# Kernel optimization log

Measured on AMD Instinct MI355X. Metric: run time of the kernel, lower is better.

The kernel has to match this reference:

```python
import jax, jax.numpy as jnp
import numpy as np

B, N, D, P = 4, 512, 512, 128

def setup_inputs() -> dict:
    key = jax.random.key(0)
    ks = jax.random.split(key, 8)
    s = lambda fan_in: 1.0 / np.sqrt(fan_in)
    inp = {
        "input": jax.random.normal(ks[0], (B, N, D), dtype=jnp.float32),
        # bigram projections (weights stored [in, out]; torch Linear is [out, in])
        "Wl": jax.random.uniform(ks[1], (D, P), jnp.float32, -s(D), s(D)),
        "bl": jnp.zeros((P,), jnp.float32),  # zeroed in initialize_parameters
        "Wr": jax.random.uniform(ks[2], (D, P), jnp.float32, -s(D), s(D)),  # no bias
        "Wo": jax.random.uniform(ks[3], (P, 1), jnp.float32, -s(P), s(P)),
        "bo": jnp.zeros((1,), jnp.float32),
        # start builder MLP
        "Ws1": jax.random.uniform(ks[4], (D, P), jnp.float32, -s(D), s(D)),
        "bs1": jnp.zeros((P,), jnp.float32),
        "Ws2": jax.random.uniform(ks[5], (P, 1), jnp.float32, -s(P), s(P)),
        "bs2": jnp.zeros((1,), jnp.float32),
        # end builder MLP
        "We1": jax.random.uniform(ks[6], (D, P), jnp.float32, -s(D), s(D)),
        "be1": jnp.zeros((P,), jnp.float32),
        "We2": jax.random.uniform(ks[7], (P, 1), jnp.float32, -s(P), s(P)),
        "be2": jnp.zeros((1,), jnp.float32),
    }
    return inp


def reference(input, Wl, bl, Wr, Wo, bo, Ws1, bs1, Ws2, bs2, We1, be1, We2, be2):
    # start / end unigram scores: [B, N, 1]
    start = jnp.maximum(input @ Ws1 + bs1, 0.0) @ Ws2 + bs2
    end = jnp.maximum(input @ We1 + be1, 0.0) @ We2 + be2
    # bigram scores
    left = input @ Wl + bl   # [B, N, P]
    right = input @ Wr       # [B, N, P]
    # left.unsqueeze(1) + right.unsqueeze(2) -> [B, N, N, P]
    proj = left[:, None, :, :] + right[:, :, None, :]
    bigram = jnp.maximum(proj, 0.0) @ Wo + bo  # [B, N, N, 1]
    return (bigram, start, end)
```

## Files before the change

kernel.cpp:

```cpp
#include <hip/hip_runtime.h>

typedef unsigned short ushort_t;
using f32x4  = __attribute__((ext_vector_type(4))) float;
using bf16x8 = __attribute__((ext_vector_type(8))) short;
using u16x8  = __attribute__((ext_vector_type(8))) unsigned short;
using h2v    = __attribute__((ext_vector_type(2))) _Float16;

constexpr int Bc = 4;
constexpr int Nc = 512;
constexpr int Dc = 512;
constexpr int Pc = 128;
constexpr int ROWS = Bc * Nc;

__device__ inline unsigned short f2bf(float f) {
    unsigned u = __builtin_bit_cast(unsigned, f);
    unsigned r = u + 0x7fffu + ((u >> 16) & 1u);
    return (unsigned short)(r >> 16);
}

__device__ inline void gload_lds16(const void* g, void* l) {
    __builtin_amdgcn_global_load_lds(
        (const __attribute__((address_space(1))) unsigned int*)g,
        (__attribute__((address_space(3))) unsigned int*)l, 16, 0, 0);
}

__device__ inline unsigned packh2(float a, float b) {
    unsigned short lo = __builtin_bit_cast(unsigned short, (_Float16)a);
    unsigned short hi = __builtin_bit_cast(unsigned short, (_Float16)b);
    return (unsigned)lo | ((unsigned)hi << 16);
}

__global__ __launch_bounds__(256) void wconv_kernel(
    const float* __restrict__ Wl,  const float* __restrict__ Wr,
    const float* __restrict__ Ws1, const float* __restrict__ We1,
    ushort_t* __restrict__ WcatT2)
{
    const int bx = blockIdx.x, t = threadIdx.x;
    __shared__ float T[64][68];

    const int nt = bx >> 3, ks = bx & 7;
    const int mi = nt >> 1, cm0 = (nt & 1) * 64;
    const float* Wm = (mi == 0) ? Wl : (mi == 1) ? Wr : (mi == 2) ? Ws1 : We1;

    const int kk_ = t >> 4, cc = (t & 15) << 2;
    #pragma unroll
    for (int u = 0; u < 4; ++u)
        *(float4*)&T[kk_ + 16 * u][cc] =
            *(const float4*)&Wm[(size_t)(ks * 64 + kk_ + 16 * u) * Pc + cm0 + cc];
    __syncthreads();

    const int col = t & 63, c2 = t >> 6;
    #pragma unroll
    for (int h = 0; h < 2; ++h) {
        const int kc = c2 + h * 4;
        u16x8 o;
        #pragma unroll
        for (int i = 0; i < 8; ++i) o[i] = f2bf(T[kc * 8 + i][col]);
        *(u16x8*)(WcatT2 + ((size_t)(nt * 8 + ks) * 8 + kc) * 512 + col * 8) = o;
    }
}

__global__ __launch_bounds__(256) void mfma_proj4(
    const float* __restrict__ input, const ushort_t* __restrict__ WcatT2,
    const float* __restrict__ bl,
    const float* __restrict__ bs1, const float* __restrict__ Ws2,
    const float* __restrict__ be1, const float* __restrict__ We2,
    ushort_t* __restrict__ leftH, ushort_t* __restrict__ rightH,
    float* __restrict__ parts)
{
    const int mt2 = blockIdx.x, ny = blockIdx.y;
    const int row0 = mt2 * 32;
    const int t = threadIdx.x, w = t >> 6, l = t & 63;
    const int wm = w & 1, wn = w >> 1;
    const int fr = l & 15, fg = l >> 4;

    __shared__ ushort_t As[2][2048];
    __shared__ ushort_t Bs[2][4096];
    __shared__ float red[64];

    const ushort_t* Bbase = WcatT2 + (size_t)ny * 8 * 4096;

    const int sr = t >> 3, skc = t & 7;
    const float* Ain = input + (size_t)(row0 + sr) * Dc + skc * 8;
    ushort_t* Ad0 = &As[0][skc * 256 + sr * 8];
    ushort_t* Ad1 = &As[1][skc * 256 + sr * 8];

    f32x4 acc0 = {0.f, 0.f, 0.f, 0.f}, acc1 = {0.f, 0.f, 0.f, 0.f};

    float4 aE0, aE1, aO0, aO1;

#define ALOAD(P0, P1, KS)                                     \
    {                                                         \
        const float* s_ = Ain + (KS) * 64;                    \
        P0 = *(const float4*)s_;                              \
        P1 = *(const float4*)(s_ + 4);                        \
    }

#define AWRITE(DST, P0, P1)                                   \
    {                                                         \
        u16x8 o_;                                             \
        o_[0] = f2bf(P0.x); o_[1] = f2bf(P0.y);               \
        o_[2] = f2bf(P0.z); o_[3] = f2bf(P0.w);               \
        o_[4] = f2bf(P1.x); o_[5] = f2bf(P1.y);               \
        o_[6] = f2bf(P1.z); o_[7] = f2bf(P1.w);               \
        *(u16x8*)(DST) = o_;                                  \
    }

#define BSTAGE(BI, KS)                                                   \
    {                                                                    \
        const ushort_t* gb = Bbase + (KS) * 4096;                        \
        gload_lds16(gb + w * 512 + l * 8, &Bs[BI][w * 512]);             \
        gload_lds16(gb + (w + 4) * 512 + l * 8, &Bs[BI][(w + 4) * 512]); \
    }

#define COMPUTE(BI)                                                           \
    {                                                                         \
        _Pragma("unroll") for (int kk = 0; kk < 2; ++kk) {                    \
            const int kc = kk * 4 + fg;                                       \
            bf16x8 a  = *(const bf16x8*)&As[BI][kc * 256 + (wm * 16 + fr) * 8];       \
            bf16x8 b0 = *(const bf16x8*)&Bs[BI][kc * 512 + (wn * 32 + fr) * 8];       \
            bf16x8 b1 = *(const bf16x8*)&Bs[BI][kc * 512 + (wn * 32 + 16 + fr) * 8];  \
            acc0 = __builtin_amdgcn_mfma_f32_16x16x32_bf16(a, b0, acc0, 0, 0, 0);     \
            acc1 = __builtin_amdgcn_mfma_f32_16x16x32_bf16(a, b1, acc1, 0, 0, 0);     \
        }                                                                     \
    }

    ALOAD(aE0, aE1, 0);
    BSTAGE(0, 0);
    AWRITE(Ad0, aE0, aE1);
    ALOAD(aO0, aO1, 1);
    __syncthreads();

    #pragma unroll
    for (int ks2 = 0; ks2 < 8; ks2 += 2) {
        BSTAGE(1, ks2 + 1);
        if (ks2 + 2 < 8) ALOAD(aE0, aE1, ks2 + 2);
        COMPUTE(0);
        AWRITE(Ad1, aO0, aO1);
        __syncthreads();
        if (ks2 + 2 < 8) {
            BSTAGE(0, ks2 + 2);
            if (ks2 + 3 < 8) ALOAD(aO0, aO1, ks2 + 3);
        }
        COMPUTE(1);
        if (ks2 + 2 < 8) AWRITE(Ad0, aE0, aE1);
        __syncthreads();
    }
#undef ALOAD
#undef AWRITE
#undef BSTAGE
#undef COMPUTE

    const int fq4 = fg << 2;
    if (ny < 4) {
        ushort_t* outp = (ny < 2) ? leftH : rightH;
        const int cb = (ny & 1) * 64 + wn * 32;
        #pragma unroll
        for (int n = 0; n < 2; ++n) {
            const int col = cb + n * 16 + fr;
            const float bv = (ny < 2) ? bl[col] : 0.f;
            const f32x4 av = n ? acc1 : acc0;
            #pragma unroll
            for (int q = 0; q < 4; ++q) {
                float v = av[q] + bv;
                outp[(size_t)(row0 + wm * 16 + fq4 + q) * Pc + col] =
                    __builtin_bit_cast(ushort_t, (_Float16)v);
            }
        }
    } else {
        const int pi = ny - 4;
        const float* b1 = (ny < 6) ? bs1 : be1;
        const float* W2 = (ny < 6) ? Ws2 : We2;
        const int pb = (pi & 1) * 64;
        #pragma unroll
        for (int q = 0; q < 4; ++q) {
            const int cp0 = pb + wn * 32 + fr;
            const int cp1 = pb + wn * 32 + 16 + fr;
            float v = fmaxf(acc0[q] + b1[cp0], 0.f) * W2[cp0]
                    + fmaxf(acc1[q] + b1[cp1], 0.f) * W2[cp1];
            v += __shfl_xor(v, 1);
            v += __shfl_xor(v, 2);
            v += __shfl_xor(v, 4);
            v += __shfl_xor(v, 8);
            if (fr == 0) red[wn * 32 + wm * 16 + fq4 + q] = v;
        }
        __syncthreads();
        if (t < 32) parts[pi * ROWS + row0 + t] = red[t] + red[32 + t];
    }
}

__global__ __launch_bounds__(256) void bigram_kernel(
    const ushort_t* __restrict__ leftH, const ushort_t* __restrict__ rightH,
    const float* __restrict__ Wo,   const float* __restrict__ bo,
    const float* __restrict__ parts,
    const float* __restrict__ bs2,  const float* __restrict__ be2,
    float* __restrict__ out, float* __restrict__ start_out,
    float* __restrict__ end_out)
{
    const int jt = blockIdx.x, it = blockIdx.y, b = blockIdx.z;
    const int t  = threadIdx.x;

    if (jt == 16) {
        const int base = (b * 8 + it) * 64;
        if (t < 64) {
            const int r = base + t;
            start_out[r] = parts[r] + parts[ROWS + r] + bs2[0];
        } else if (t < 128) {
            const int r = base + t - 64;
            end_out[r] = parts[2 * ROWS + r] + parts[3 * ROWS + r] + be2[0];
        }
        return;
    }

    __shared__ unsigned Lh[32][68];
    __shared__ unsigned Rh[64][68];
    __shared__ unsigned woh[64];

    const ushort_t* lp = leftH  + (size_t)(b * Nc + jt * 32) * Pc;
    const ushort_t* rp = rightH + (size_t)(b * Nc + it * 64) * Pc;

    #pragma unroll
    for (int u = 0; u < 2; ++u) {
        int f = t + u * 256, r = f >> 4, c = f & 15;
        *(float4*)&Lh[r][c * 4] = *(const float4*)(lp + (size_t)r * Pc + c * 8);
    }
    #pragma unroll
    for (int u = 0; u < 4; ++u) {
        int f = t + u * 256, r = f >> 4, c = f & 15;
        *(float4*)&Rh[r][c * 4] = *(const float4*)(rp + (size_t)r * Pc + c * 8);
    }
    if (t < 64) woh[t] = packh2(Wo[2 * t], Wo[2 * t + 1]);
    __syncthreads();

    const int jl = t & 15;
    const int il = t >> 4;

    float acc[4][2] = {};
    const h2v hz = {(_Float16)0.f, (_Float16)0.f};

#define DOTH(COMP)                                                       \
    {                                                                    \
        const unsigned wu = w4.COMP;                                     \
        h2v lv[2], rv[4];                                                \
        lv[0] = __builtin_bit_cast(h2v, l4[0].COMP);                     \
        lv[1] = __builtin_bit_cast(h2v, l4[1].COMP);                     \
        rv[0] = __builtin_bit_cast(h2v, r4[0].COMP);                     \
        rv[1] = __builtin_bit_cast(h2v, r4[1].COMP);                     \
        rv[2] = __builtin_bit_cast(h2v, r4[2].COMP);                     \
        rv[3] = __builtin_bit_cast(h2v, r4[3].COMP);                     \
        _Pragma("unroll") for (int ii = 0; ii < 4; ++ii)                 \
        _Pragma("unroll") for (int jj = 0; jj < 2; ++jj) {               \
            h2v sum = lv[jj] + rv[ii];                                   \
            sum = __builtin_elementwise_max(sum, hz);                    \
            unsigned su = __builtin_bit_cast(unsigned, sum);             \
            asm("v_dot2_f32_f16 %0, %1, %2, %0"                          \
                : "+v"(acc[ii][jj]) : "v"(su), "v"(wu));                 \
        }                                                                \
    }

    #pragma unroll 4
    for (int s4 = 0; s4 < 16; ++s4) {
        uint4 w4 = *(const uint4*)&woh[4 * s4];
        uint4 l4[2], r4[4];
        #pragma unroll
        for (int jj = 0; jj < 2; ++jj) l4[jj] = *(const uint4*)&Lh[jl + 16 * jj][4 * s4];
        #pragma unroll
        for (int ii = 0; ii < 4; ++ii) r4[ii] = *(const uint4*)&Rh[il + 16 * ii][4 * s4];
        DOTH(x) DOTH(y) DOTH(z) DOTH(w)
    }
#undef DOTH

    const float bias = bo[0];
    #pragma unroll
    for (int ii = 0; ii < 4; ++ii) {
        #pragma unroll
        for (int jj = 0; jj < 2; ++jj) {
            const int gi = it * 64 + il + 16 * ii;
            const int gj = jt * 32 + jl + 16 * jj;
            out[((size_t)b * Nc + gi) * Nc + gj] = acc[ii][jj] + bias;
        }
    }
}

extern "C" void kernel_launch(void* const* d_in, const int* in_sizes, int n_in,
                              void* d_out, int out_size, void* d_ws, size_t ws_size,
                              hipStream_t stream) {
    const float* input = (const float*)d_in[0];
    const float* Wl  = (const float*)d_in[1];
    const float* bl  = (const float*)d_in[2];
    const float* Wr  = (const float*)d_in[3];
    const float* Wo  = (const float*)d_in[4];
    const float* bo  = (const float*)d_in[5];
    const float* Ws1 = (const float*)d_in[6];
    const float* bs1 = (const float*)d_in[7];
    const float* Ws2 = (const float*)d_in[8];
    const float* bs2 = (const float*)d_in[9];
    const float* We1 = (const float*)d_in[10];
    const float* be1 = (const float*)d_in[11];
    const float* We2 = (const float*)d_in[12];
    const float* be2 = (const float*)d_in[13];

    float* out    = (float*)d_out;
    float* bigram = out;
    float* start  = out + (size_t)Bc * Nc * Nc;
    float* end    = start + (size_t)Bc * Nc;

    ushort_t* leftH  = (ushort_t*)d_ws;
    ushort_t* rightH = leftH + (size_t)ROWS * Pc;
    float* parts     = (float*)(rightH + (size_t)ROWS * Pc);
    ushort_t* WcatT2 = (ushort_t*)(parts + 4 * ROWS);

    wconv_kernel<<<64, 256, 0, stream>>>(Wl, Wr, Ws1, We1, WcatT2);

    mfma_proj4<<<dim3(64, 8), 256, 0, stream>>>(
        input, WcatT2, bl, bs1, Ws2, be1, We2, leftH, rightH, parts);

    bigram_kernel<<<dim3(17, 8, 4), 256, 0, stream>>>(
        leftH, rightH, Wo, bo, parts, bs2, be2, bigram, start, end);
}
```

Before: 31.37 us.

## Enlarge bigram tile to 64x64 and double-buffer LDS register loads

Each bigram block now covers 64 j columns instead of 32, so each thread computes a 4x4 accumulator tile and the grid halves in x. Per-step LDS operands are loaded into two alternating register sets, so the next step's loads are issued before the current step's dot products. The inline-asm dot2 is replaced with the fdot2 builtin. The larger tile reuses LDS reads more per thread and halves the number of blocks (288 instead of 544), at the cost of more registers and less parallelism to hide latency.

```diff
diff --git a/kernel.cpp b/kernel.cpp
--- a/kernel.cpp
+++ b/kernel.cpp
@@ -86,7 +86,6 @@
     ushort_t* Ad1 = &As[1][skc * 256 + sr * 8];
 
     f32x4 acc0 = {0.f, 0.f, 0.f, 0.f}, acc1 = {0.f, 0.f, 0.f, 0.f};
-
     float4 aE0, aE1, aO0, aO1;
 
 #define ALOAD(P0, P1, KS)                                     \
@@ -200,7 +199,7 @@
     const int jt = blockIdx.x, it = blockIdx.y, b = blockIdx.z;
     const int t  = threadIdx.x;
 
-    if (jt == 16) {
+    if (jt == 8) {
         const int base = (b * 8 + it) * 64;
         if (t < 64) {
             const int r = base + t;
@@ -212,15 +211,15 @@
         return;
     }
 
-    __shared__ unsigned Lh[32][68];
+    __shared__ unsigned Lh[64][68];
     __shared__ unsigned Rh[64][68];
     __shared__ unsigned woh[64];
 
-    const ushort_t* lp = leftH  + (size_t)(b * Nc + jt * 32) * Pc;
+    const ushort_t* lp = leftH  + (size_t)(b * Nc + jt * 64) * Pc;
     const ushort_t* rp = rightH + (size_t)(b * Nc + it * 64) * Pc;
 
     #pragma unroll
-    for (int u = 0; u < 2; ++u) {
+    for (int u = 0; u < 4; ++u) {
         int f = t + u * 256, r = f >> 4, c = f & 15;
         *(float4*)&Lh[r][c * 4] = *(const float4*)(lp + (size_t)r * Pc + c * 8);
     }
@@ -235,48 +234,63 @@
     const int jl = t & 15;
     const int il = t >> 4;
 
-    float acc[4][2] = {};
+    float acc[4][4] = {};
     const h2v hz = {(_Float16)0.f, (_Float16)0.f};
 
-#define DOTH(COMP)                                                       \
+#define LOADP(S, W4, L4, R4)                                             \
     {                                                                    \
-        const unsigned wu = w4.COMP;                                     \
-        h2v lv[2], rv[4];                                                \
-        lv[0] = __builtin_bit_cast(h2v, l4[0].COMP);                     \
-        lv[1] = __builtin_bit_cast(h2v, l4[1].COMP);                     \
-        rv[0] = __builtin_bit_cast(h2v, r4[0].COMP);                     \
-        rv[1] = __builtin_bit_cast(h2v, r4[1].COMP);                     \
-        rv[2] = __builtin_bit_cast(h2v, r4[2].COMP);                     \
-        rv[3] = __builtin_bit_cast(h2v, r4[3].COMP);                     \
+        W4 = *(const uint4*)&woh[4 * (S)];                               \
+        _Pragma("unroll") for (int jj = 0; jj < 4; ++jj)                 \
+            L4[jj] = *(const uint4*)&Lh[jl + 16 * jj][4 * (S)];          \
         _Pragma("unroll") for (int ii = 0; ii < 4; ++ii)                 \
-        _Pragma("unroll") for (int jj = 0; jj < 2; ++jj) {               \
+            R4[ii] = *(const uint4*)&Rh[il + 16 * ii][4 * (S)];          \
+    }
+
+#define COMP1(W4, L4, R4, C)                                             \
+    {                                                                    \
+        const h2v wv = __builtin_bit_cast(h2v, W4.C);                    \
+        h2v lv[4] = {__builtin_bit_cast(h2v, L4[0].C),                   \
+                     __builtin_bit_cast(h2v, L4[1].C),                   \
+                     __builtin_bit_cast(h2v, L4[2].C),                   \
+                     __builtin_bit_cast(h2v, L4[3].C)};                  \
+        h2v rv[4] = {__builtin_bit_cast(h2v, R4[0].C),                   \
+                     __builtin_bit_cast(h2v, R4[1].C),                   \
+                     __builtin_bit_cast(h2v, R4[2].C),                   \
+                     __builtin_bit_cast(h2v, R4[3].C)};                  \
+        _Pragma("unroll") for (int ii = 0; ii < 4; ++ii)                 \
+        _Pragma("unroll") for (int jj = 0; jj < 4; ++jj) {               \
             h2v sum = lv[jj] + rv[ii];                                   \
             sum = __builtin_elementwise_max(sum, hz);                    \
-            unsigned su = __builtin_bit_cast(unsigned, sum);             \
-            asm("v_dot2_f32_f16 %0, %1, %2, %0"                          \
-                : "+v"(acc[ii][jj]) : "v"(su), "v"(wu));                 \
+            acc[ii][jj] = __builtin_amdgcn_fdot2(sum, wv, acc[ii][jj], false); \
         }                                                                \
     }
 
-    #pragma unroll 4
-    for (int s4 = 0; s4 < 16; ++s4) {
-        uint4 w4 = *(const uint4*)&woh[4 * s4];
-        uint4 l4[2], r4[4];
-        #pragma unroll
-        for (int jj = 0; jj < 2; ++jj) l4[jj] = *(const uint4*)&Lh[jl + 16 * jj][4 * s4];
-        #pragma unroll
-        for (int ii = 0; ii < 4; ++ii) r4[ii] = *(const uint4*)&Rh[il + 16 * ii][4 * s4];
-        DOTH(x) DOTH(y) DOTH(z) DOTH(w)
-    }
-#undef DOTH
+#define COMP(W4, L4, R4)                                                 \
+    { COMP1(W4, L4, R4, x) COMP1(W4, L4, R4, y)                          \
+      COMP1(W4, L4, R4, z) COMP1(W4, L4, R4, w) }
+
+    uint4 wA, lA[4], rA[4];
+    uint4 wB, lB[4], rB[4];
+    LOADP(0, wA, lA, rA);
+
+    #pragma unroll 1
+    for (int s = 0; s < 16; s += 2) {
+        LOADP(s + 1, wB, lB, rB);
+        COMP(wA, lA, rA);
+        if (s + 2 < 16) LOADP(s + 2, wA, lA, rA);
+        COMP(wB, lB, rB);
+    }
+#undef LOADP
+#undef COMP1
+#undef COMP
 
     const float bias = bo[0];
     #pragma unroll
     for (int ii = 0; ii < 4; ++ii) {
         #pragma unroll
-        for (int jj = 0; jj < 2; ++jj) {
+        for (int jj = 0; jj < 4; ++jj) {
             const int gi = it * 64 + il + 16 * ii;
-            const int gj = jt * 32 + jl + 16 * jj;
+            const int gj = jt * 64 + jl + 16 * jj;
             out[((size_t)b * Nc + gi) * Nc + gj] = acc[ii][jj] + bias;
         }
     }
@@ -315,6 +329,6 @@
     mfma_proj4<<<dim3(64, 8), 256, 0, stream>>>(
         input, WcatT2, bl, bs1, Ws2, be1, We2, leftH, rightH, parts);
 
-    bigram_kernel<<<dim3(17, 8, 4), 256, 0, stream>>>(
+    bigram_kernel<<<dim3(9, 8, 4), 256, 0, stream>>>(
         leftH, rightH, Wo, bo, parts, bs2, be2, bigram, start, end);
 }
```

Measured after the change: 36.29 us. 1.16x slower.

## Restructure bigram kernel to hold left rows and Wo in registers per lane

Applied to the files above, without the earlier changes.

The bigram tile changes from 64 i by 32 j to 32 i by 64 j. Each lane now owns one j column and keeps that left row and the packed Wo half in registers, while each wave streams 8 right rows from LDS, which LDS can broadcast. The grid becomes 9x16x4 and the start/end finishing blocks are remapped. The aim is to cut LDS read traffic per dot product, at the cost of heavy register pressure (32 lreg, 32 wreg and 32 rreg values plus 16 accumulators) that may lower occupancy.

```diff
diff --git a/kernel.cpp b/kernel.cpp
--- a/kernel.cpp
+++ b/kernel.cpp
@@ -5,6 +5,7 @@
 using bf16x8 = __attribute__((ext_vector_type(8))) short;
 using u16x8  = __attribute__((ext_vector_type(8))) unsigned short;
 using h2v    = __attribute__((ext_vector_type(2))) _Float16;
+using u32x4  = __attribute__((ext_vector_type(4))) unsigned;
 
 constexpr int Bc = 4;
 constexpr int Nc = 512;
@@ -86,7 +87,6 @@
     ushort_t* Ad1 = &As[1][skc * 256 + sr * 8];
 
     f32x4 acc0 = {0.f, 0.f, 0.f, 0.f}, acc1 = {0.f, 0.f, 0.f, 0.f};
-
     float4 aE0, aE1, aO0, aO1;
 
 #define ALOAD(P0, P1, KS)                                     \
@@ -200,86 +200,101 @@
     const int jt = blockIdx.x, it = blockIdx.y, b = blockIdx.z;
     const int t  = threadIdx.x;
 
-    if (jt == 16) {
-        const int base = (b * 8 + it) * 64;
-        if (t < 64) {
-            const int r = base + t;
-            start_out[r] = parts[r] + parts[ROWS + r] + bs2[0];
-        } else if (t < 128) {
-            const int r = base + t - 64;
-            end_out[r] = parts[2 * ROWS + r] + parts[3 * ROWS + r] + be2[0];
+    if (jt == 8) {
+        if (it < 8) {
+            const int base = (b * 8 + it) * 64;
+            if (t < 64) {
+                const int r = base + t;
+                start_out[r] = parts[r] + parts[ROWS + r] + bs2[0];
+            } else if (t < 128) {
+                const int r = base + t - 64;
+                end_out[r] = parts[2 * ROWS + r] + parts[3 * ROWS + r] + be2[0];
+            }
         }
         return;
     }
 
-    __shared__ unsigned Lh[32][68];
-    __shared__ unsigned Rh[64][68];
-    __shared__ unsigned woh[64];
-
-    const ushort_t* lp = leftH  + (size_t)(b * Nc + jt * 32) * Pc;
-    const ushort_t* rp = rightH + (size_t)(b * Nc + it * 64) * Pc;
-
+    __shared__ unsigned Lh[64 * 68];
+    __shared__ unsigned Rh[32 * 68];
+    __shared__ unsigned woS[64];
+
+    const int lane = t & 63, w = t >> 6;
+
+    if (t < 64) woS[t] = packh2(Wo[2 * t], Wo[2 * t + 1]);
+
+    const ushort_t* lbase = leftH + ((size_t)b * Nc + jt * 64) * Pc;
+    #pragma unroll
+    for (int u = 0; u < 4; ++u) {
+        int idx = t + u * 256, row = idx >> 4, c4 = idx & 15;
+        *(u32x4*)&Lh[row * 68 + c4 * 4] =
+            *(const u32x4*)(lbase + (size_t)row * Pc + c4 * 8);
+    }
+    const ushort_t* rbase = rightH + ((size_t)b * Nc + it * 32) * Pc;
     #pragma unroll
     for (int u = 0; u < 2; ++u) {
-        int f = t + u * 256, r = f >> 4, c = f & 15;
-        *(float4*)&Lh[r][c * 4] = *(const float4*)(lp + (size_t)r * Pc + c * 8);
-    }
-    #pragma unroll
-    for (int u = 0; u < 4; ++u) {
-        int f = t + u * 256, r = f >> 4, c = f & 15;
-        *(float4*)&Rh[r][c * 4] = *(const float4*)(rp + (size_t)r * Pc + c * 8);
-    }
-    if (t < 64) woh[t] = packh2(Wo[2 * t], Wo[2 * t + 1]);
+        int idx = t + u * 256, row = idx >> 4, c4 = idx & 15;
+        *(u32x4*)&Rh[row * 68 + c4 * 4] =
+            *(const u32x4*)(rbase + (size_t)row * Pc + c4 * 8);
+    }
     __syncthreads();
 
-    const int jl = t & 15;
-    const int il = t >> 4;
-
-    float acc[4][2] = {};
+    float acc0[8] = {}, acc1[8] = {};
     const h2v hz = {(_Float16)0.f, (_Float16)0.f};
-
-#define DOTH(COMP)                                                       \
-    {                                                                    \
-        const unsigned wu = w4.COMP;                                     \
-        h2v lv[2], rv[4];                                                \
-        lv[0] = __builtin_bit_cast(h2v, l4[0].COMP);                     \
-        lv[1] = __builtin_bit_cast(h2v, l4[1].COMP);                     \
-        rv[0] = __builtin_bit_cast(h2v, r4[0].COMP);                     \
-        rv[1] = __builtin_bit_cast(h2v, r4[1].COMP);                     \
-        rv[2] = __builtin_bit_cast(h2v, r4[2].COMP);                     \
-        rv[3] = __builtin_bit_cast(h2v, r4[3].COMP);                     \
-        _Pragma("unroll") for (int ii = 0; ii < 4; ++ii)                 \
-        _Pragma("unroll") for (int jj = 0; jj < 2; ++jj) {               \
-            h2v sum = lv[jj] + rv[ii];                                   \
-            sum = __builtin_elementwise_max(sum, hz);                    \
-            unsigned su = __builtin_bit_cast(unsigned, sum);             \
-            asm("v_dot2_f32_f16 %0, %1, %2, %0"                          \
-                : "+v"(acc[ii][jj]) : "v"(su), "v"(wu));                 \
-        }                                                                \
-    }
-
-    #pragma unroll 4
-    for (int s4 = 0; s4 < 16; ++s4) {
-        uint4 w4 = *(const uint4*)&woh[4 * s4];
-        uint4 l4[2], r4[4];
-        #pragma unroll
-        for (int jj = 0; jj < 2; ++jj) l4[jj] = *(const uint4*)&Lh[jl + 16 * jj][4 * s4];
-        #pragma unroll
-        for (int ii = 0; ii < 4; ++ii) r4[ii] = *(const uint4*)&Rh[il + 16 * ii][4 * s4];
-        DOTH(x) DOTH(y) DOTH(z) DOTH(w)
-    }
-#undef DOTH
+    const unsigned* lrow = &Lh[lane * 68];
+    const unsigned* rw   = &Rh[(w * 8) * 68];
+
+    #pragma unroll
+    for (int half = 0; half < 2; ++half) {
+        const int hoff = half * 32;
+
+        unsigned lreg[32];
+        #pragma unroll
+        for (int c = 0; c < 8; ++c) {
+            u32x4 v = *(const u32x4*)&lrow[hoff + 4 * c];
+            lreg[4 * c]     = v[0]; lreg[4 * c + 1] = v[1];
+            lreg[4 * c + 2] = v[2]; lreg[4 * c + 3] = v[3];
+        }
+        unsigned wreg[32];
+        #pragma unroll
+        for (int c = 0; c < 8; ++c) {
+            u32x4 v = *(const u32x4*)&woS[hoff + 4 * c];
+            wreg[4 * c]     = v[0]; wreg[4 * c + 1] = v[1];
+            wreg[4 * c + 2] = v[2]; wreg[4 * c + 3] = v[3];
+        }
+
+        #pragma unroll
+        for (int i = 0; i < 8; ++i) {
+            unsigned rreg[32];
+            #pragma unroll
+            for (int c = 0; c < 8; ++c) {
+                u32x4 v = *(const u32x4*)&rw[i * 68 + hoff + 4 * c];
+                rreg[4 * c]     = v[0]; rreg[4 * c + 1] = v[1];
+                rreg[4 * c + 2] = v[2]; rreg[4 * c + 3] = v[3];
+            }
+            float a0 = acc0[i], a1 = acc1[i];
+            #pragma unroll
+            for (int m = 0; m < 32; m += 2) {
+                h2v s0 = __builtin_bit_cast(h2v, lreg[m])
+                       + __builtin_bit_cast(h2v, rreg[m]);
+                s0 = __builtin_elementwise_max(s0, hz);
+                a0 = __builtin_amdgcn_fdot2(
+                         s0, __builtin_bit_cast(h2v, wreg[m]), a0, false);
+                h2v s1 = __builtin_bit_cast(h2v, lreg[m + 1])
+                       + __builtin_bit_cast(h2v, rreg[m + 1]);
+                s1 = __builtin_elementwise_max(s1, hz);
+                a1 = __builtin_amdgcn_fdot2(
+                         s1, __builtin_bit_cast(h2v, wreg[m + 1]), a1, false);
+            }
+            acc0[i] = a0; acc1[i] = a1;
+        }
+    }
 
     const float bias = bo[0];
-    #pragma unroll
-    for (int ii = 0; ii < 4; ++ii) {
-        #pragma unroll
-        for (int jj = 0; jj < 2; ++jj) {
-            const int gi = it * 64 + il + 16 * ii;
-            const int gj = jt * 32 + jl + 16 * jj;
-            out[((size_t)b * Nc + gi) * Nc + gj] = acc[ii][jj] + bias;
-        }
-    }
+    const int gi0 = it * 32 + w * 8;
+    const int gj  = jt * 64 + lane;
+    #pragma unroll
+    for (int i = 0; i < 8; ++i)
+        out[((size_t)b * Nc + gi0 + i) * Nc + gj] = acc0[i] + acc1[i] + bias;
 }
 
 extern "C" void kernel_launch(void* const* d_in, const int* in_sizes, int n_in,
@@ -315,6 +330,6 @@
     mfma_proj4<<<dim3(64, 8), 256, 0, stream>>>(
         input, WcatT2, bl, bs1, Ws2, be1, We2, leftH, rightH, parts);
 
-    bigram_kernel<<<dim3(17, 8, 4), 256, 0, stream>>>(
+    bigram_kernel<<<dim3(9, 16, 4), 256, 0, stream>>>(
         leftH, rightH, Wo, bo, parts, bs2, be2, bigram, start, end);
 }
```

Result: no change. 31.04 us (-1.0%).
